# Optimization experiments

Measured on AMD Instinct MI355X. Metric: run time of the kernel, lower is better.

Reference implementation:

```python
import jax, jax.numpy as jnp
import numpy as np

BETA = 0.25  # commitment loss weight


def setup_inputs() -> dict:
    key = jax.random.key(0)
    k1, k2 = jax.random.split(key)
    x = jax.random.normal(k1, (16, 2048, 512), dtype=jnp.float32)          # [B, T, D]
    codebooks = jax.random.normal(k2, (8, 1024, 512), dtype=jnp.float32)   # [Q, C, D]
    return {"x": x, "codebooks": codebooks}


def reference(x, codebooks):
    """Residual VQ (SoundStream Algorithm 1): per stage, find nearest codebook
    entry to the current residual (squared-L2 cdist + argmin), gather the code,
    accumulate into the quantized output, subtract from the residual.
    Straight-through estimator on the quantize step; beta-weighted commit loss.
    """

    def step(carry, embed):
        residual, quantized_out, loss = carry  # residual: [B,T,D], embed: [C,D]
        # squared distances ||r - e||^2, GEMM-dominated: [B,T,C]
        d2 = (jnp.sum(residual * residual, axis=-1, keepdims=True)
              - 2.0 * jnp.einsum('btd,cd->btc', residual, embed)
              + jnp.sum(embed * embed, axis=-1))
        idx = jnp.argmin(d2, axis=-1)                 # [B,T] int32
        quant = embed[idx]                            # [B,T,D] gather
        # straight-through: forward value = quant, gradient = identity to residual
        quant_st = residual + jax.lax.stop_gradient(quant - residual)
        loss = loss + BETA * jnp.mean((residual - jax.lax.stop_gradient(quant)) ** 2)
        return (residual - quant_st, quantized_out + quant_st, loss), idx

    init = (x, jnp.zeros_like(x), jnp.float32(0.0))
    (_, quantized_out, loss), all_indices = jax.lax.scan(step, init, codebooks)
    # quantized_out: [B,T,D]; all_indices: [Q,B,T]; loss: scalar
    return quantized_out, all_indices, loss
```

## Files before the change

### kernel.cpp

```cpp
#include <hip/hip_runtime.h>

#define B_   16
#define T_   2048
#define D_   512
#define C_   1024
#define Q_   8
#define M_   (B_ * T_)
#define ND_  (M_ * D_)

static constexpr float BETA = 0.25f;

typedef short  short8v __attribute__((ext_vector_type(8)));
typedef short  short4v __attribute__((ext_vector_type(4)));
typedef float  f32x4   __attribute__((ext_vector_type(4)));

#define WS_CB16     0u
#define WS_ENORM    8388608u
#define WS_IDXI     8421376u
#define WS_FLAGS    8552448u
#define WS_CNT      8683520u
#define WS_NEED1    8683552u
#define WS_CB16LO   8683552u
#define WS_NEED2    17072160u
#define WS_CBT      17072384u
#define WS_NEED3    19169536u
#define WS_NEED3ALL 33849600u

__device__ __forceinline__ short f2bf(float f) {
    unsigned u = __float_as_uint(f);
    u += 0x7fffu + ((u >> 16) & 1u);
    return (short)(u >> 16);
}
__device__ __forceinline__ float bf2f(short s) {
    return __uint_as_float(((unsigned)(unsigned short)s) << 16);
}

__global__ __launch_bounds__(256) void k_enorm(const float* __restrict__ cb,
                                               float* __restrict__ enorm) {
    const int wave = threadIdx.x >> 6;
    const int lane = threadIdx.x & 63;
    const int code = blockIdx.x * 4 + wave;
    const float4* row = (const float4*)(cb + (size_t)code * D_);
    float s = 0.f;
    #pragma unroll
    for (int k = 0; k < 2; ++k) {
        float4 v = row[lane + k * 64];
        s += v.x * v.x + v.y * v.y + v.z * v.z + v.w * v.w;
    }
    #pragma unroll
    for (int m = 32; m; m >>= 1) s += __shfl_xor(s, m);
    if (lane == 0) enorm[code] = s;
}

__global__ __launch_bounds__(256) void k_cvt2f(const float* __restrict__ cb,
                                               short* __restrict__ hi,
                                               short* __restrict__ lo,
                                               int emit_lo) {
    const int idx8 = blockIdx.x * 256 + threadIdx.x;
    const int stage = idx8 >> 16;
    const int g = idx8 & 65535;
    const int lane = g & 63;
    const int h  = lane >> 4, lr = lane & 15;
    const int cj = (g >> 6) & 3;
    const int wc = (g >> 8) & 3;
    const int kb = (g >> 10) & 15;
    const int cc = (g >> 14) & 3;
    const int c  = cc * 256 + wc * 64 + cj * 16 + lr;
    const int ks = kb * 32 + h * 8;
    const float* src = cb + (size_t)stage * (C_ * D_) + (size_t)c * D_ + ks;
    float v[8];
    {
        float4 a = *(const float4*)(src);
        float4 b = *(const float4*)(src + 4);
        v[0]=a.x; v[1]=a.y; v[2]=a.z; v[3]=a.w;
        v[4]=b.x; v[5]=b.y; v[6]=b.z; v[7]=b.w;
    }
    short8v hv, lv;
    #pragma unroll
    for (int k = 0; k < 8; ++k) {
        hv[k] = f2bf(v[k]);
        lv[k] = f2bf(v[k] - bf2f(hv[k]));
    }
    const size_t dst = (size_t)stage * (C_ * D_) + (size_t)g * 8;
    *(short8v*)(hi + dst) = hv;
    if (emit_lo) *(short8v*)(lo + dst) = lv;
}

__global__ __launch_bounds__(64) void k_zero(float* __restrict__ loss,
                                             int* __restrict__ cnt) {
    if (threadIdx.x == 0) *loss = 0.f;
    if (threadIdx.x < 8) cnt[threadIdx.x] = 0;
}

__global__ __launch_bounds__(256)
void k_transpose(const float* __restrict__ cb0, float* __restrict__ cbT0) {
    __shared__ float tile[64][65];
    const float* cbq = cb0 + (size_t)blockIdx.z * C_ * D_;
    float* cbT = cbT0 + (size_t)blockIdx.z * C_ * D_;
    const int tid = threadIdx.x;
    const int c0 = blockIdx.x * 64;
    const int k0 = blockIdx.y * 64;
    #pragma unroll
    for (int i = 0; i < 4; ++i) {
        const int s = tid + i * 256;
        const int r = s >> 4, c4 = s & 15;
        const float4 v = *(const float4*)(cbq + (size_t)(c0 + r) * D_ + k0 + c4 * 4);
        tile[r][c4 * 4 + 0] = v.x; tile[r][c4 * 4 + 1] = v.y;
        tile[r][c4 * 4 + 2] = v.z; tile[r][c4 * 4 + 3] = v.w;
    }
    __syncthreads();
    #pragma unroll
    for (int i = 0; i < 4; ++i) {
        const int s = tid + i * 256;
        const int kk = s >> 4, cc4 = s & 15;
        float4 v;
        v.x = tile[cc4 * 4 + 0][kk]; v.y = tile[cc4 * 4 + 1][kk];
        v.z = tile[cc4 * 4 + 2][kk]; v.w = tile[cc4 * 4 + 3][kk];
        *(float4*)(cbT + (size_t)(k0 + kk) * C_ + c0 + cc4 * 4) = v;
    }
}

#define SA_OFF   0
#define MV1_OFF  131072
#define MV2_OFF  133120
#define MI1_OFF  135168
#define RED_OFF  137216
#define MROW_OFF 137248
#define SM_TOTAL 137760

template <int PLANES>
__global__ __launch_bounds__(512, 2)
void k_approx(const float* __restrict__ x,
              const float* __restrict__ cbprev,
              const short* __restrict__ cb16hi,
              const short* __restrict__ cb16lo,
              const float* __restrict__ enormq,
              float* __restrict__ qout,
              int*   __restrict__ idxi,
              float* __restrict__ idxf,
              int*   __restrict__ flaglist,
              int*   __restrict__ cnt,
              float* __restrict__ loss,
              int q) {
    __shared__ __align__(16) char smem[SM_TOTAL];
    short* smA  = (short*)(smem + SA_OFF);
    float* mv1  = (float*)(smem + MV1_OFF);
    float* mv2  = (float*)(smem + MV2_OFF);
    int*   mi1  = (int*)(smem + MI1_OFF);
    float* red  = (float*)(smem + RED_OFF);
    float* mrow = (float*)(smem + MROW_OFF);

    const int tid  = threadIdx.x;
    const int bid  = blockIdx.x;
    const int lane = tid & 63;
    const int w    = tid >> 6;
    const int rh   = w >> 2;
    const int wc   = w & 3;
    const int h    = lane >> 4;
    const int lr   = lane & 15;
    const int rbase = bid * 128;
    const float slope = (PLANES == 2) ? 0.002f : 0.05f;

    const int prow = tid >> 2;
    const int pqd  = tid & 3;
    const int grow1 = rbase + prow;
    float rn2 = 0.f, rlo2 = 0.f;
    int codep = 0;
    if (q > 0) codep = idxi[grow1];
    #pragma unroll 4
    for (int j = 0; j < 32; ++j) {
        const int c4 = pqd + j * 4;
        const size_t g = (size_t)grow1 * D_ + c4 * 4;
        const float4 xv = *(const float4*)(x + g);
        float4 r;
        if (q == 0) {
            r = xv;
        } else {
            const float4 ev = *(const float4*)(cbprev + (size_t)codep * D_ + c4 * 4);
            float4 nq;
            if (q == 1) nq = ev;
            else {
                const float4 qv = *(const float4*)(qout + g);
                nq = make_float4(qv.x + ev.x, qv.y + ev.y, qv.z + ev.z, qv.w + ev.w);
            }
            *(float4*)(qout + g) = nq;
            r = make_float4(xv.x - nq.x, xv.y - nq.y, xv.z - nq.z, xv.w - nq.w);
        }
        rn2 += r.x * r.x + r.y * r.y + r.z * r.z + r.w * r.w;
        short4v sv; sv[0]=f2bf(r.x); sv[1]=f2bf(r.y); sv[2]=f2bf(r.z); sv[3]=f2bf(r.w);
        const float dx = r.x - bf2f(sv[0]), dy = r.y - bf2f(sv[1]);
        const float dz = r.z - bf2f(sv[2]), dw = r.w - bf2f(sv[3]);
        rlo2 += dx * dx + dy * dy + dz * dz + dw * dw;
        int ab = (prow << 10) + (c4 << 3);
        ab ^= ((prow & 7) << 4);
        *(short4v*)((char*)smA + ab) = sv;
    }
    const float lpart = rn2;
    rn2  += __shfl_xor(rn2, 1);  rn2  += __shfl_xor(rn2, 2);
    rlo2 += __shfl_xor(rlo2, 1); rlo2 += __shfl_xor(rlo2, 2);
    if (pqd == 0)
        mrow[prow] = 32.f * sqrtf(rlo2) + slope * sqrtf(rn2) + 0.05f;
    __syncthreads();
    if (q != 0) {
        float lsum = lpart;
        #pragma unroll
        for (int m = 32; m; m >>= 1) lsum += __shfl_xor(lsum, m);
        if (lane == 0) red[w] = lsum;
        __syncthreads();
        if (tid == 0) {
            float t = 0.f;
            #pragma unroll
            for (int i = 0; i < 8; ++i) t += red[i];
            atomicAdd(loss, t * (BETA / (float)ND_));
        }
    }

    float v1[16], v2[16]; int i1[16];
    #pragma unroll
    for (int i = 0; i < 16; ++i) { v1[i] = 3.4e38f; v2[i] = 3.4e38f; i1[i] = 0; }

    auto bload = [&](const short* __restrict__ src, int cc, int kb, short8v* dst) {
        const short* p = src + (size_t)(((cc * 16 + kb) * 4 + wc) * 4) * 512 + lane * 8;
        #pragma unroll
        for (int cj = 0; cj < 4; ++cj)
            dst[cj] = *(const short8v*)(p + cj * 512);
    };

    short8v b0[4], b1[4];
    bload(cb16hi, 0, 0, b0);
    f32x4 acc[4][4];

    for (int cc = 0; cc < 4; ++cc) {
        #pragma unroll
        for (int ri = 0; ri < 4; ++ri)
            #pragma unroll
            for (int cj = 0; cj < 4; ++cj)
                acc[ri][cj] = (f32x4){0.f, 0.f, 0.f, 0.f};

        if (PLANES == 2) {
            for (int kb = 0; kb < 16; ++kb) {
                bload(cb16lo, cc, kb, b1);
                short8v a[4];
                const int kbyte = kb * 64 + h * 16;
                #pragma unroll
                for (int ri = 0; ri < 4; ++ri) {
                    const int row = rh * 64 + ri * 16 + lr;
                    int off = (row << 10) + kbyte;
                    off ^= ((row & 7) << 4);
                    a[ri] = *(const short8v*)((const char*)smA + off);
                }
                #pragma unroll
                for (int ri = 0; ri < 4; ++ri)
                    #pragma unroll
                    for (int cj = 0; cj < 4; ++cj)
                        acc[ri][cj] = __builtin_amdgcn_mfma_f32_16x16x32_bf16(a[ri], b0[cj], acc[ri][cj], 0, 0, 0);
                const int nkb = (kb == 15) ? 0 : kb + 1;
                const int ncc = (kb == 15) ? (cc < 3 ? cc + 1 : 3) : cc;
                bload(cb16hi, ncc, nkb, b0);
                #pragma unroll
                for (int ri = 0; ri < 4; ++ri)
                    #pragma unroll
                    for (int cj = 0; cj < 4; ++cj)
                        acc[ri][cj] = __builtin_amdgcn_mfma_f32_16x16x32_bf16(a[ri], b1[cj], acc[ri][cj], 0, 0, 0);
            }
        } else {
            for (int kb = 0; kb < 16; kb += 2) {
                {
                    short8v a[4];
                    const int kbyte = kb * 64 + h * 16;
                    #pragma unroll
                    for (int ri = 0; ri < 4; ++ri) {
                        const int row = rh * 64 + ri * 16 + lr;
                        int off = (row << 10) + kbyte;
                        off ^= ((row & 7) << 4);
                        a[ri] = *(const short8v*)((const char*)smA + off);
                    }
                    bload(cb16hi, cc, kb + 1, b1);
                    #pragma unroll
                    for (int ri = 0; ri < 4; ++ri)
                        #pragma unroll
                        for (int cj = 0; cj < 4; ++cj)
                            acc[ri][cj] = __builtin_amdgcn_mfma_f32_16x16x32_bf16(a[ri], b0[cj], acc[ri][cj], 0, 0, 0);
                }
                {
                    short8v a[4];
                    const int kbyte = (kb + 1) * 64 + h * 16;
                    #pragma unroll
                    for (int ri = 0; ri < 4; ++ri) {
                        const int row = rh * 64 + ri * 16 + lr;
                        int off = (row << 10) + kbyte;
                        off ^= ((row & 7) << 4);
                        a[ri] = *(const short8v*)((const char*)smA + off);
                    }
                    const int nkb = (kb == 14) ? 0 : kb + 2;
                    const int ncc = (kb == 14) ? (cc < 3 ? cc + 1 : 3) : cc;
                    bload(cb16hi, ncc, nkb, b0);
                    #pragma unroll
                    for (int ri = 0; ri < 4; ++ri)
                        #pragma unroll
                        for (int cj = 0; cj < 4; ++cj)
                            acc[ri][cj] = __builtin_amdgcn_mfma_f32_16x16x32_bf16(a[ri], b1[cj], acc[ri][cj], 0, 0, 0);
                }
            }
        }

        #pragma unroll
        for (int cj = 0; cj < 4; ++cj) {
            const int codeG = cc * 256 + wc * 64 + cj * 16 + lr;
            const float en = enormq[codeG];
            #pragma unroll
            for (int ri = 0; ri < 4; ++ri)
                #pragma unroll
                for (int rg = 0; rg < 4; ++rg) {
                    const float sv = fmaf(-2.f, acc[ri][cj][rg], en);
                    const int slot = ri * 4 + rg;
                    if (sv < v1[slot]) { v2[slot] = v1[slot]; v1[slot] = sv; i1[slot] = codeG; }
                    else               { v2[slot] = fminf(v2[slot], sv); }
                }
        }
    }

    #pragma unroll
    for (int slot = 0; slot < 16; ++slot) {
        float a1 = v1[slot], a2 = v2[slot]; int ai = i1[slot];
        #pragma unroll
        for (int m = 1; m < 16; m <<= 1) {
            const float b1m = __shfl_xor(a1, m);
            const int   bim = __shfl_xor(ai, m);
            const float b2m = __shfl_xor(a2, m);
            if (b1m < a1 || (b1m == a1 && bim < ai)) { a2 = fminf(a1, b2m); a1 = b1m; ai = bim; }
            else                                     { a2 = fminf(a2, b1m); }
        }
        v1[slot] = a1; v2[slot] = a2; i1[slot] = ai;
    }
    if (lr == 0) {
        #pragma unroll
        for (int ri = 0; ri < 4; ++ri)
            #pragma unroll
            for (int rg = 0; rg < 4; ++rg) {
                const int row = rh * 64 + ri * 16 + h * 4 + rg;
                mv1[wc * 128 + row] = v1[ri * 4 + rg];
                mv2[wc * 128 + row] = v2[ri * 4 + rg];
                mi1[wc * 128 + row] = i1[ri * 4 + rg];
            }
    }
    __syncthreads();

    if (tid < 128) {
        const int row = tid;
        float V1 = mv1[row]; int I1 = mi1[row]; float V2 = mv2[row];
        #pragma unroll
        for (int k = 1; k < 4; ++k) {
            const float b1m = mv1[k * 128 + row];
            const int   bim = mi1[k * 128 + row];
            const float b2m = mv2[k * 128 + row];
            if (b1m < V1 || (b1m == V1 && bim < I1)) { V2 = fminf(V1, b2m); V1 = b1m; I1 = bim; }
            else                                     { V2 = fminf(V2, b1m); }
        }
        const int grow = rbase + row;
        idxi[grow] = I1;
        idxf[grow] = (float)I1;
        if (!(V2 - V1 >= mrow[row])) {
            const int p = atomicAdd(cnt, 1);
            flaglist[p] = grow;
        }
    }
}

__global__ __launch_bounds__(256, 1)
void k_exact_t(const float* __restrict__ x, const float* __restrict__ qout,
               const float* __restrict__ cbT, const float* __restrict__ enq,
               int* __restrict__ idxi, float* __restrict__ idxf,
               const int* __restrict__ flaglist, const int* __restrict__ cnt,
               int useq) {
    __shared__ __align__(16) float rr[8][512];
    __shared__ int   rowid[8];
    __shared__ float wvv[8][4];
    __shared__ int   wii[8][4];
    const int tid  = threadIdx.x;
    const int lane = tid & 63;
    const int wv_  = tid >> 6;
    const int n = *cnt;
    const float4* cbT4 = (const float4*)cbT;

    for (int base = blockIdx.x * 8; base < n; base += gridDim.x * 8) {
        __syncthreads();
        if (tid < 8) rowid[tid] = (base + tid < n) ? flaglist[base + tid] : -1;
        __syncthreads();
        #pragma unroll
        for (int i = 0; i < 4; ++i) {
            const int s = tid + i * 256;
            const int j = s >> 7, k4 = s & 127;
            const int row = rowid[j];
            float4 v = make_float4(0.f, 0.f, 0.f, 0.f);
            if (row >= 0) {
                v = *(const float4*)(x + (size_t)row * D_ + k4 * 4);
                if (useq) {
                    const float4 qv = *(const float4*)(qout + (size_t)row * D_ + k4 * 4);
                    v = make_float4(v.x - qv.x, v.y - qv.y, v.z - qv.z, v.w - qv.w);
                }
            }
            *(float4*)&rr[j][k4 * 4] = v;
        }
        __syncthreads();

        float acc[8][4];
        #pragma unroll
        for (int j = 0; j < 8; ++j)
            #pragma unroll
            for (int c = 0; c < 4; ++c) acc[j][c] = 0.f;

        auto load16 = [&](float4* buf, int k0) {
            #pragma unroll
            for (int t = 0; t < 16; ++t)
                buf[t] = cbT4[(size_t)(k0 + t) * 256 + tid];
        };
        auto compute16 = [&](const float4* buf, int k0) {
            #pragma unroll
            for (int g = 0; g < 4; ++g) {
                const float4 e0 = buf[g * 4 + 0], e1 = buf[g * 4 + 1];
                const float4 e2 = buf[g * 4 + 2], e3 = buf[g * 4 + 3];
                #pragma unroll
                for (int j = 0; j < 8; ++j) {
                    const float4 rv = *(const float4*)&rr[j][k0 + g * 4];
                    acc[j][0] = fmaf(rv.x, e0.x, acc[j][0]);
                    acc[j][1] = fmaf(rv.x, e0.y, acc[j][1]);
                    acc[j][2] = fmaf(rv.x, e0.z, acc[j][2]);
                    acc[j][3] = fmaf(rv.x, e0.w, acc[j][3]);
                    acc[j][0] = fmaf(rv.y, e1.x, acc[j][0]);
                    acc[j][1] = fmaf(rv.y, e1.y, acc[j][1]);
                    acc[j][2] = fmaf(rv.y, e1.z, acc[j][2]);
                    acc[j][3] = fmaf(rv.y, e1.w, acc[j][3]);
                    acc[j][0] = fmaf(rv.z, e2.x, acc[j][0]);
                    acc[j][1] = fmaf(rv.z, e2.y, acc[j][1]);
                    acc[j][2] = fmaf(rv.z, e2.z, acc[j][2]);
                    acc[j][3] = fmaf(rv.z, e2.w, acc[j][3]);
                    acc[j][0] = fmaf(rv.w, e3.x, acc[j][0]);
                    acc[j][1] = fmaf(rv.w, e3.y, acc[j][1]);
                    acc[j][2] = fmaf(rv.w, e3.z, acc[j][2]);
                    acc[j][3] = fmaf(rv.w, e3.w, acc[j][3]);
                }
            }
        };

        float4 bufA[16], bufB[16];
        load16(bufA, 0);
        for (int ss = 0; ss < 32; ss += 2) {
            load16(bufB, (ss + 1) * 16);
            compute16(bufA, ss * 16);
            if (ss + 2 < 32) load16(bufA, (ss + 2) * 16);
            compute16(bufB, (ss + 1) * 16);
        }

        const float4 en4 = *(const float4*)(enq + tid * 4);
        #pragma unroll
        for (int j = 0; j < 8; ++j) {
            float v = 3.4e38f; int id = 0;
            {
                const float s0 = fmaf(-2.f, acc[j][0], en4.x);
                const float s1 = fmaf(-2.f, acc[j][1], en4.y);
                const float s2 = fmaf(-2.f, acc[j][2], en4.z);
                const float s3 = fmaf(-2.f, acc[j][3], en4.w);
                v = s0; id = tid * 4;
                if (s1 < v) { v = s1; id = tid * 4 + 1; }
                if (s2 < v) { v = s2; id = tid * 4 + 2; }
                if (s3 < v) { v = s3; id = tid * 4 + 3; }
            }
            #pragma unroll
            for (int m = 1; m < 64; m <<= 1) {
                const float ov = __shfl_xor(v, m);
                const int  oid = __shfl_xor(id, m);
                if (ov < v || (ov == v && oid < id)) { v = ov; id = oid; }
            }
            if (lane == 0) { wvv[j][wv_] = v; wii[j][wv_] = id; }
        }
        __syncthreads();
        if (tid < 8 && rowid[tid] >= 0) {
            float V = wvv[tid][0]; int I = wii[tid][0];
            #pragma unroll
            for (int k = 1; k < 4; ++k)
                if (wvv[tid][k] < V || (wvv[tid][k] == V && wii[tid][k] < I)) {
                    V = wvv[tid][k]; I = wii[tid][k];
                }
            idxi[rowid[tid]] = I;
            idxf[rowid[tid]] = (float)I;
        }
    }
}

#define XR 4
__global__ __launch_bounds__(256)
void k_exact(const float* __restrict__ x, const float* __restrict__ qout,
             const float* __restrict__ cbq, const float* __restrict__ enq,
             int* __restrict__ idxi, float* __restrict__ idxf,
             const int* __restrict__ flaglist, const int* __restrict__ cnt,
             int useq) {
    __shared__ float rr[XR][512];
    __shared__ int   rowid[XR];
    __shared__ float wv[4];
    __shared__ int   wi[4];
    const int tid = threadIdx.x;
    const int n = *cnt;
    for (int base = blockIdx.x * XR; base < n; base += gridDim.x * XR) {
        __syncthreads();
        if (tid < XR) rowid[tid] = (base + tid < n) ? flaglist[base + tid] : -1;
        __syncthreads();
        #pragma unroll
        for (int i = 0; i < 8; ++i) {
            const int s = tid + i * 256;
            const int j = s >> 9, k = s & 511;
            const int row = rowid[j];
            float v = 0.f;
            if (row >= 0) {
                v = x[(size_t)row * D_ + k];
                if (useq) v -= qout[(size_t)row * D_ + k];
            }
            rr[j][k] = v;
        }
        __syncthreads();
        float dotv[4][XR];
        #pragma unroll
        for (int cs = 0; cs < 4; ++cs)
            #pragma unroll
            for (int j = 0; j < XR; ++j) dotv[cs][j] = 0.f;
        for (int k4 = 0; k4 < 128; ++k4) {
            float4 rv[XR];
            #pragma unroll
            for (int j = 0; j < XR; ++j) rv[j] = *(const float4*)&rr[j][k4 * 4];
            #pragma unroll
            for (int cs = 0; cs < 4; ++cs) {
                const float4 e = *(const float4*)(cbq + (size_t)(cs * 256 + tid) * D_ + k4 * 4);
                #pragma unroll
                for (int j = 0; j < XR; ++j)
                    dotv[cs][j] = fmaf(e.x, rv[j].x, fmaf(e.y, rv[j].y,
                                  fmaf(e.z, rv[j].z, fmaf(e.w, rv[j].w, dotv[cs][j]))));
            }
        }
        float best[XR]; int bidx[XR];
        #pragma unroll
        for (int j = 0; j < XR; ++j) { best[j] = 3.4e38f; bidx[j] = 0; }
        #pragma unroll
        for (int cs = 0; cs < 4; ++cs) {
            const int c = cs * 256 + tid;
            const float en = enq[c];
            #pragma unroll
            for (int j = 0; j < XR; ++j) {
                const float sc = fmaf(-2.f, dotv[cs][j], en);
                if (sc < best[j]) { best[j] = sc; bidx[j] = c; }
            }
        }
        #pragma unroll
        for (int j = 0; j < XR; ++j) {
            float v = best[j]; int id = bidx[j];
            #pragma unroll
            for (int m = 1; m < 64; m <<= 1) {
                const float ov = __shfl_xor(v, m);
                const int  oid = __shfl_xor(id, m);
                if (ov < v || (ov == v && oid < id)) { v = ov; id = oid; }
            }
            if ((tid & 63) == 0) { wv[tid >> 6] = v; wi[tid >> 6] = id; }
            __syncthreads();
            if (tid == 0 && rowid[j] >= 0) {
                float V = wv[0]; int I = wi[0];
                #pragma unroll
                for (int k = 1; k < 4; ++k)
                    if (wv[k] < V || (wv[k] == V && wi[k] < I)) { V = wv[k]; I = wi[k]; }
                idxi[rowid[j]] = I;
                idxf[rowid[j]] = (float)I;
            }
            __syncthreads();
        }
    }
}

__global__ __launch_bounds__(256)
void k_final(const float* __restrict__ x, const float* __restrict__ cb7,
             const int* __restrict__ idxi, float* __restrict__ qout,
             float* __restrict__ loss) {
    __shared__ float red[4];
    const int tid = threadIdx.x;
    const int rbase = blockIdx.x * 64;
    float lsum = 0.f;
    for (int i = 0; i < 32; ++i) {
        const int s = tid + i * 256;
        const int row = s >> 7, c4 = s & 127;
        const int grow = rbase + row;
        const int code = idxi[grow];
        const float4 ev = *(const float4*)(cb7 + (size_t)code * D_ + c4 * 4);
        const size_t g = (size_t)grow * D_ + c4 * 4;
        const float4 xv = *(const float4*)(x + g);
        const float4 qv = *(const float4*)(qout + g);
        const float4 nq = make_float4(qv.x + ev.x, qv.y + ev.y, qv.z + ev.z, qv.w + ev.w);
        *(float4*)(qout + g) = nq;
        const float rx = xv.x - nq.x, ry = xv.y - nq.y;
        const float rz = xv.z - nq.z, rw = xv.w - nq.w;
        lsum += rx * rx + ry * ry + rz * rz + rw * rw;
    }
    #pragma unroll
    for (int m = 32; m; m >>= 1) lsum += __shfl_xor(lsum, m);
    if ((tid & 63) == 0) red[tid >> 6] = lsum;
    __syncthreads();
    if (tid == 0)
        atomicAdd(loss, (red[0] + red[1] + red[2] + red[3]) * (BETA / (float)ND_));
}

__global__ __launch_bounds__(256) void k_init(float* __restrict__ qout,
                                              float* __restrict__ loss) {
    const size_t tid = (size_t)blockIdx.x * blockDim.x + threadIdx.x;
    float4* q4 = (float4*)qout;
    const size_t n4 = ND_ / 4;
    for (size_t i = tid; i < n4; i += (size_t)gridDim.x * blockDim.x)
        q4[i] = make_float4(0.f, 0.f, 0.f, 0.f);
    if (tid == 0) *loss = 0.f;
}

__global__ __launch_bounds__(256) void k_stage(const float* __restrict__ x,
                                               const float* __restrict__ cb,
                                               const float* __restrict__ enorm,
                                               float* __restrict__ qout,
                                               float* __restrict__ idxf,
                                               float* __restrict__ loss) {
    __shared__ float As[16][68];
    __shared__ float Bs[16][68];
    __shared__ int   sidx[64];
    __shared__ float red[4];
    const int tid = threadIdx.x;
    const int ty  = tid >> 4;
    const int tx  = tid & 15;
    const int rbase = blockIdx.x * 64;
    const int lrow = tid >> 2;
    const int ld4  = tid & 3;
    float minv[4]; int mini[4];
    #pragma unroll
    for (int i = 0; i < 4; ++i) { minv[i] = 3.4e38f; mini[i] = 0; }
    for (int cchunk = 0; cchunk < 16; ++cchunk) {
        const int cbase = cchunk * 64;
        float acc[4][4] = {};
        for (int kb = 0; kb < D_; kb += 16) {
            __syncthreads();
            {
                const size_t g = (size_t)(rbase + lrow) * D_ + kb + ld4 * 4;
                const float4 xv = *(const float4*)(x + g);
                const float4 qv = *(const float4*)(qout + g);
                As[ld4*4+0][lrow] = xv.x - qv.x; As[ld4*4+1][lrow] = xv.y - qv.y;
                As[ld4*4+2][lrow] = xv.z - qv.z; As[ld4*4+3][lrow] = xv.w - qv.w;
                const size_t gb = (size_t)(cbase + lrow) * D_ + kb + ld4 * 4;
                const float4 bv = *(const float4*)(cb + gb);
                Bs[ld4*4+0][lrow] = bv.x; Bs[ld4*4+1][lrow] = bv.y;
                Bs[ld4*4+2][lrow] = bv.z; Bs[ld4*4+3][lrow] = bv.w;
            }
            __syncthreads();
            #pragma unroll
            for (int kk = 0; kk < 16; ++kk) {
                const float4 av = *(const float4*)&As[kk][ty * 4];
                const float4 bv = *(const float4*)&Bs[kk][tx * 4];
                const float a[4] = {av.x, av.y, av.z, av.w};
                const float b[4] = {bv.x, bv.y, bv.z, bv.w};
                #pragma unroll
                for (int i = 0; i < 4; ++i)
                    #pragma unroll
                    for (int j = 0; j < 4; ++j)
                        acc[i][j] = fmaf(a[i], b[j], acc[i][j]);
            }
        }
        #pragma unroll
        for (int j = 0; j < 4; ++j) {
            const int c = cbase + tx * 4 + j;
            const float en = enorm[c];
            #pragma unroll
            for (int i = 0; i < 4; ++i) {
                const float s = fmaf(-2.f, acc[i][j], en);
                if (s < minv[i]) { minv[i] = s; mini[i] = c; }
            }
        }
    }
    #pragma unroll
    for (int i = 0; i < 4; ++i) {
        float v = minv[i]; int id = mini[i];
        #pragma unroll
        for (int m = 1; m < 16; m <<= 1) {
            const float ov = __shfl_xor(v, m); const int oid = __shfl_xor(id, m);
            if (ov < v || (ov == v && oid < id)) { v = ov; id = oid; }
        }
        if (tx == 0) sidx[ty * 4 + i] = id;
    }
    __syncthreads();
    if (tid < 64) idxf[rbase + tid] = (float)sidx[tid];
    float lsum = 0.f;
    #pragma unroll 4
    for (int k = 0; k < 32; ++k) {
        const int fidx = tid + k * 256;
        const int row = fidx >> 7, c4 = fidx & 127;
        const int code = sidx[row];
        const float4 qv = *(const float4*)(cb + (size_t)code * D_ + c4 * 4);
        const size_t g = (size_t)(rbase + row) * D_ + c4 * 4;
        const float4 xv = *(const float4*)(x + g);
        const float4 ov = *(const float4*)(qout + g);
        const float4 nq = make_float4(ov.x + qv.x, ov.y + qv.y, ov.z + qv.z, ov.w + qv.w);
        *(float4*)(qout + g) = nq;
        const float rx = xv.x - nq.x, ry = xv.y - nq.y;
        const float rz = xv.z - nq.z, rw = xv.w - nq.w;
        lsum += rx * rx + ry * ry + rz * rz + rw * rw;
    }
    #pragma unroll
    for (int m = 32; m; m >>= 1) lsum += __shfl_xor(lsum, m);
    if ((tid & 63) == 0) red[tid >> 6] = lsum;
    __syncthreads();
    if (tid == 0)
        atomicAdd(loss, (red[0] + red[1] + red[2] + red[3]) * (BETA / (float)ND_));
}

extern "C" void kernel_launch(void* const* d_in, const int* in_sizes, int n_in,
                              void* d_out, int out_size, void* d_ws, size_t ws_size,
                              hipStream_t stream) {
    const float* x  = (const float*)d_in[0];
    const float* cb = (const float*)d_in[1];

    float* out  = (float*)d_out;
    float* qout = out;
    float* idxf = out + (size_t)ND_;
    float* loss = out + (size_t)ND_ + (size_t)Q_ * M_;

    if (ws_size >= WS_NEED1) {
        const bool twop   = (ws_size >= WS_NEED2);
        const bool hascbt = (ws_size >= WS_NEED3);
        const bool hasall = (ws_size >= WS_NEED3ALL);
        char*  ws    = (char*)d_ws;
        short* cb16  = (short*)(ws + WS_CB16);
        short* cb16l = (short*)(ws + WS_CB16LO);
        float* enorm = (float*)(ws + WS_ENORM);
        int*   idxi  = (int*)(ws + WS_IDXI);
        int*   flags = (int*)(ws + WS_FLAGS);
        int*   cnt   = (int*)(ws + WS_CNT);
        float* cbT   = (float*)(ws + WS_CBT);

        hipLaunchKernelGGL(k_zero, dim3(1), dim3(64), 0, stream, loss, cnt);
        hipLaunchKernelGGL(k_cvt2f, dim3(2048), dim3(256), 0, stream,
                           cb, cb16, twop ? cb16l : cb16, twop ? 1 : 0);
        hipLaunchKernelGGL(k_enorm, dim3((Q_ * C_) / 4), dim3(256), 0, stream, cb, enorm);
        if (hasall)
            hipLaunchKernelGGL(k_transpose, dim3(16, 8, 8), dim3(256), 0, stream, cb, cbT);

        for (int q = 0; q < Q_; ++q) {
            if (twop) {
                hipLaunchKernelGGL((k_approx<2>), dim3(M_ / 128), dim3(512), 0, stream,
                                   x, cb + (size_t)(q > 0 ? q - 1 : 0) * C_ * D_,
                                   cb16 + (size_t)q * C_ * D_,
                                   cb16l + (size_t)q * C_ * D_,
                                   enorm + (size_t)q * C_,
                                   qout, idxi, idxf + (size_t)q * M_,
                                   flags, cnt + q, loss, q);
            } else {
                hipLaunchKernelGGL((k_approx<1>), dim3(M_ / 128), dim3(512), 0, stream,
                                   x, cb + (size_t)(q > 0 ? q - 1 : 0) * C_ * D_,
                                   cb16 + (size_t)q * C_ * D_,
                                   cb16 + (size_t)q * C_ * D_,
                                   enorm + (size_t)q * C_,
                                   qout, idxi, idxf + (size_t)q * M_,
                                   flags, cnt + q, loss, q);
            }
            if (hascbt) {
                if (!hasall)
                    hipLaunchKernelGGL(k_transpose, dim3(16, 8, 1), dim3(256), 0, stream,
                                       cb + (size_t)q * C_ * D_, cbT);
                hipLaunchKernelGGL(k_exact_t, dim3(512), dim3(256), 0, stream,
                                   x, qout,
                                   hasall ? (cbT + (size_t)q * C_ * D_) : cbT,
                                   enorm + (size_t)q * C_,
                                   idxi, idxf + (size_t)q * M_,
                                   flags, cnt + q, q > 0 ? 1 : 0);
            } else {
                hipLaunchKernelGGL(k_exact, dim3(512), dim3(256), 0, stream,
                                   x, qout,
                                   cb + (size_t)q * C_ * D_,
                                   enorm + (size_t)q * C_,
                                   idxi, idxf + (size_t)q * M_,
                                   flags, cnt + q, q > 0 ? 1 : 0);
            }
        }
        hipLaunchKernelGGL(k_final, dim3(M_ / 64), dim3(256), 0, stream,
                           x, cb + (size_t)(Q_ - 1) * C_ * D_, idxi, qout, loss);
    } else {
        float* enorm = (float*)d_ws;
        hipLaunchKernelGGL(k_init, dim3(4096), dim3(256), 0, stream, qout, loss);
        hipLaunchKernelGGL(k_enorm, dim3((Q_ * C_) / 4), dim3(256), 0, stream, cb, enorm);
        for (int q = 0; q < Q_; ++q) {
            hipLaunchKernelGGL(k_stage, dim3(M_ / 64), dim3(256), 0, stream,
                               x, cb + (size_t)q * C_ * D_, enorm + (size_t)q * C_,
                               qout, idxf + (size_t)q * M_, loss);
        }
    }
}
```

Before: 1.537 ms.

## Replace two-plane bf16 distance GEMM with single-plane fp16 MFMA

The approximate distance pass switches from bf16 hi+lo split codebooks (two MFMA passes per k-block) to a single fp16 codebook plane and fp16 MFMA, halving the MFMA work and B-operand traffic. The candidate margin formula is retuned for fp16 rounding error so that fewer rows should be flagged for exact recompute. The exact fallback kernel's register double-buffer shrinks from 16 to 8 float4 per buffer and drops its occupancy bound. The risk is fp16 overflow or precision loss on large residuals, which would flag more rows for exact rescoring.

```diff
diff --git a/kernel.cpp b/kernel.cpp
--- a/kernel.cpp
+++ b/kernel.cpp
@@ -10,9 +10,11 @@
 
 static constexpr float BETA = 0.25f;
 
-typedef short  short8v __attribute__((ext_vector_type(8)));
-typedef short  short4v __attribute__((ext_vector_type(4)));
-typedef float  f32x4   __attribute__((ext_vector_type(4)));
+typedef short    short8v __attribute__((ext_vector_type(8)));
+typedef short    short4v __attribute__((ext_vector_type(4)));
+typedef _Float16 half8v  __attribute__((ext_vector_type(8)));
+typedef _Float16 half4v  __attribute__((ext_vector_type(4)));
+typedef float    f32x4   __attribute__((ext_vector_type(4)));
 
 #define WS_CB16     0u
 #define WS_ENORM    8388608u
@@ -20,20 +22,9 @@
 #define WS_FLAGS    8552448u
 #define WS_CNT      8683520u
 #define WS_NEED1    8683552u
-#define WS_CB16LO   8683552u
-#define WS_NEED2    17072160u
-#define WS_CBT      17072384u
-#define WS_NEED3    19169536u
-#define WS_NEED3ALL 33849600u
-
-__device__ __forceinline__ short f2bf(float f) {
-    unsigned u = __float_as_uint(f);
-    u += 0x7fffu + ((u >> 16) & 1u);
-    return (short)(u >> 16);
-}
-__device__ __forceinline__ float bf2f(short s) {
-    return __uint_as_float(((unsigned)(unsigned short)s) << 16);
-}
+#define WS_CBT      8683552u
+#define WS_NEED2    10780704u
+#define WS_NEED2ALL 25460768u
 
 __global__ __launch_bounds__(256) void k_enorm(const float* __restrict__ cb,
                                                float* __restrict__ enorm) {
@@ -52,10 +43,8 @@
     if (lane == 0) enorm[code] = s;
 }
 
-__global__ __launch_bounds__(256) void k_cvt2f(const float* __restrict__ cb,
-                                               short* __restrict__ hi,
-                                               short* __restrict__ lo,
-                                               int emit_lo) {
+__global__ __launch_bounds__(256) void k_cvtf16(const float* __restrict__ cb,
+                                                short* __restrict__ hi) {
     const int idx8 = blockIdx.x * 256 + threadIdx.x;
     const int stage = idx8 >> 16;
     const int g = idx8 & 65535;
@@ -75,15 +64,11 @@
         v[0]=a.x; v[1]=a.y; v[2]=a.z; v[3]=a.w;
         v[4]=b.x; v[5]=b.y; v[6]=b.z; v[7]=b.w;
     }
-    short8v hv, lv;
-    #pragma unroll
-    for (int k = 0; k < 8; ++k) {
-        hv[k] = f2bf(v[k]);
-        lv[k] = f2bf(v[k] - bf2f(hv[k]));
-    }
+    half8v hv;
+    #pragma unroll
+    for (int k = 0; k < 8; ++k) hv[k] = (_Float16)v[k];
     const size_t dst = (size_t)stage * (C_ * D_) + (size_t)g * 8;
-    *(short8v*)(hi + dst) = hv;
-    if (emit_lo) *(short8v*)(lo + dst) = lv;
+    *(half8v*)(hi + dst) = hv;
 }
 
 __global__ __launch_bounds__(64) void k_zero(float* __restrict__ loss,
@@ -128,12 +113,10 @@
 #define MROW_OFF 137248
 #define SM_TOTAL 137760
 
-template <int PLANES>
 __global__ __launch_bounds__(512, 2)
 void k_approx(const float* __restrict__ x,
               const float* __restrict__ cbprev,
-              const short* __restrict__ cb16hi,
-              const short* __restrict__ cb16lo,
+              const short* __restrict__ cb16,
               const float* __restrict__ enormq,
               float* __restrict__ qout,
               int*   __restrict__ idxi,
@@ -159,7 +142,6 @@
     const int h    = lane >> 4;
     const int lr   = lane & 15;
     const int rbase = bid * 128;
-    const float slope = (PLANES == 2) ? 0.002f : 0.05f;
 
     const int prow = tid >> 2;
     const int pqd  = tid & 3;
@@ -187,19 +169,21 @@
             r = make_float4(xv.x - nq.x, xv.y - nq.y, xv.z - nq.z, xv.w - nq.w);
         }
         rn2 += r.x * r.x + r.y * r.y + r.z * r.z + r.w * r.w;
-        short4v sv; sv[0]=f2bf(r.x); sv[1]=f2bf(r.y); sv[2]=f2bf(r.z); sv[3]=f2bf(r.w);
-        const float dx = r.x - bf2f(sv[0]), dy = r.y - bf2f(sv[1]);
-        const float dz = r.z - bf2f(sv[2]), dw = r.w - bf2f(sv[3]);
+        half4v hv;
+        hv[0] = (_Float16)r.x; hv[1] = (_Float16)r.y;
+        hv[2] = (_Float16)r.z; hv[3] = (_Float16)r.w;
+        const float dx = r.x - (float)hv[0], dy = r.y - (float)hv[1];
+        const float dz = r.z - (float)hv[2], dw = r.w - (float)hv[3];
         rlo2 += dx * dx + dy * dy + dz * dz + dw * dw;
         int ab = (prow << 10) + (c4 << 3);
         ab ^= ((prow & 7) << 4);
-        *(short4v*)((char*)smA + ab) = sv;
+        *(half4v*)((char*)smA + ab) = hv;
     }
     const float lpart = rn2;
     rn2  += __shfl_xor(rn2, 1);  rn2  += __shfl_xor(rn2, 2);
     rlo2 += __shfl_xor(rlo2, 1); rlo2 += __shfl_xor(rlo2, 2);
     if (pqd == 0)
-        mrow[prow] = 32.f * sqrtf(rlo2) + slope * sqrtf(rn2) + 0.05f;
+        mrow[prow] = 18.f * sqrtf(rlo2) + 0.005f * sqrtf(rn2) + 0.05f;
     __syncthreads();
     if (q != 0) {
         float lsum = lpart;
@@ -227,7 +211,7 @@
     };
 
     short8v b0[4], b1[4];
-    bload(cb16hi, 0, 0, b0);
+    bload(cb16, 0, 0, b0);
     f32x4 acc[4][4];
 
     for (int cc = 0; cc < 4; ++cc) {
@@ -237,9 +221,8 @@
             for (int cj = 0; cj < 4; ++cj)
                 acc[ri][cj] = (f32x4){0.f, 0.f, 0.f, 0.f};
 
-        if (PLANES == 2) {
-            for (int kb = 0; kb < 16; ++kb) {
-                bload(cb16lo, cc, kb, b1);
+        for (int kb = 0; kb < 16; kb += 2) {
+            {
                 short8v a[4];
                 const int kbyte = kb * 64 + h * 16;
                 #pragma unroll
@@ -249,58 +232,33 @@
                     off ^= ((row & 7) << 4);
                     a[ri] = *(const short8v*)((const char*)smA + off);
                 }
+                bload(cb16, cc, kb + 1, b1);
                 #pragma unroll
                 for (int ri = 0; ri < 4; ++ri)
                     #pragma unroll
                     for (int cj = 0; cj < 4; ++cj)
-                        acc[ri][cj] = __builtin_amdgcn_mfma_f32_16x16x32_bf16(a[ri], b0[cj], acc[ri][cj], 0, 0, 0);
-                const int nkb = (kb == 15) ? 0 : kb + 1;
-                const int ncc = (kb == 15) ? (cc < 3 ? cc + 1 : 3) : cc;
-                bload(cb16hi, ncc, nkb, b0);
+                        acc[ri][cj] = __builtin_amdgcn_mfma_f32_16x16x32_f16(
+                            *(half8v*)&a[ri], *(half8v*)&b0[cj], acc[ri][cj], 0, 0, 0);
+            }
+            {
+                short8v a[4];
+                const int kbyte = (kb + 1) * 64 + h * 16;
+                #pragma unroll
+                for (int ri = 0; ri < 4; ++ri) {
+                    const int row = rh * 64 + ri * 16 + lr;
+                    int off = (row << 10) + kbyte;
+                    off ^= ((row & 7) << 4);
+                    a[ri] = *(const short8v*)((const char*)smA + off);
+                }
+                const int nkb = (kb == 14) ? 0 : kb + 2;
+                const int ncc = (kb == 14) ? (cc < 3 ? cc + 1 : 3) : cc;
+                bload(cb16, ncc, nkb, b0);
                 #pragma unroll
                 for (int ri = 0; ri < 4; ++ri)
                     #pragma unroll
                     for (int cj = 0; cj < 4; ++cj)
-                        acc[ri][cj] = __builtin_amdgcn_mfma_f32_16x16x32_bf16(a[ri], b1[cj], acc[ri][cj], 0, 0, 0);
-            }
-        } else {
-            for (int kb = 0; kb < 16; kb += 2) {
-                {
-                    short8v a[4];
-                    const int kbyte = kb * 64 + h * 16;
-                    #pragma unroll
-                    for (int ri = 0; ri < 4; ++ri) {
-                        const int row = rh * 64 + ri * 16 + lr;
-                        int off = (row << 10) + kbyte;
-                        off ^= ((row & 7) << 4);
-                        a[ri] = *(const short8v*)((const char*)smA + off);
-                    }
-                    bload(cb16hi, cc, kb + 1, b1);
-                    #pragma unroll
-                    for (int ri = 0; ri < 4; ++ri)
-                        #pragma unroll
-                        for (int cj = 0; cj < 4; ++cj)
-                            acc[ri][cj] = __builtin_amdgcn_mfma_f32_16x16x32_bf16(a[ri], b0[cj], acc[ri][cj], 0, 0, 0);
-                }
-                {
-                    short8v a[4];
-                    const int kbyte = (kb + 1) * 64 + h * 16;
-                    #pragma unroll
-                    for (int ri = 0; ri < 4; ++ri) {
-                        const int row = rh * 64 + ri * 16 + lr;
-                        int off = (row << 10) + kbyte;
-                        off ^= ((row & 7) << 4);
-                        a[ri] = *(const short8v*)((const char*)smA + off);
-                    }
-                    const int nkb = (kb == 14) ? 0 : kb + 2;
-                    const int ncc = (kb == 14) ? (cc < 3 ? cc + 1 : 3) : cc;
-                    bload(cb16hi, ncc, nkb, b0);
-                    #pragma unroll
-                    for (int ri = 0; ri < 4; ++ri)
-                        #pragma unroll
-                        for (int cj = 0; cj < 4; ++cj)
-                            acc[ri][cj] = __builtin_amdgcn_mfma_f32_16x16x32_bf16(a[ri], b1[cj], acc[ri][cj], 0, 0, 0);
-                }
+                        acc[ri][cj] = __builtin_amdgcn_mfma_f32_16x16x32_f16(
+                            *(half8v*)&a[ri], *(half8v*)&b1[cj], acc[ri][cj], 0, 0, 0);
             }
         }
 
@@ -367,12 +325,12 @@
     }
 }
 
-__global__ __launch_bounds__(256, 1)
-void k_exact_t(const float* __restrict__ x, const float* __restrict__ qout,
-               const float* __restrict__ cbT, const float* __restrict__ enq,
-               int* __restrict__ idxi, float* __restrict__ idxf,
-               const int* __restrict__ flaglist, const int* __restrict__ cnt,
-               int useq) {
+__global__ __launch_bounds__(256)
+void k_exact3(const float* __restrict__ x, const float* __restrict__ qout,
+              const float* __restrict__ cbT, const float* __restrict__ enq,
+              int* __restrict__ idxi, float* __restrict__ idxf,
+              const int* __restrict__ flaglist, const int* __restrict__ cnt,
+              int useq) {
     __shared__ __align__(16) float rr[8][512];
     __shared__ int   rowid[8];
     __shared__ float wvv[8][4];
@@ -410,19 +368,21 @@
             #pragma unroll
             for (int c = 0; c < 4; ++c) acc[j][c] = 0.f;
 
-        auto load16 = [&](float4* buf, int k0) {
-            #pragma unroll
-            for (int t = 0; t < 16; ++t)
-                buf[t] = cbT4[(size_t)(k0 + t) * 256 + tid];
-        };
-        auto compute16 = [&](const float4* buf, int k0) {
-            #pragma unroll
-            for (int g = 0; g < 4; ++g) {
-                const float4 e0 = buf[g * 4 + 0], e1 = buf[g * 4 + 1];
-                const float4 e2 = buf[g * 4 + 2], e3 = buf[g * 4 + 3];
+        float4 bufA[8], bufB[8];
+        #pragma unroll
+        for (int t = 0; t < 8; ++t) bufA[t] = cbT4[(size_t)t * 256 + tid];
+
+        for (int g = 0; g < 64; g += 2) {
+            const int k0 = g * 8;
+            #pragma unroll
+            for (int t = 0; t < 8; ++t) bufB[t] = cbT4[(size_t)(k0 + 8 + t) * 256 + tid];
+            #pragma unroll
+            for (int kk = 0; kk < 8; kk += 4) {
                 #pragma unroll
                 for (int j = 0; j < 8; ++j) {
-                    const float4 rv = *(const float4*)&rr[j][k0 + g * 4];
+                    const float4 rv = *(const float4*)&rr[j][k0 + kk];
+                    const float4 e0 = bufA[kk + 0], e1 = bufA[kk + 1];
+                    const float4 e2 = bufA[kk + 2], e3 = bufA[kk + 3];
                     acc[j][0] = fmaf(rv.x, e0.x, acc[j][0]);
                     acc[j][1] = fmaf(rv.x, e0.y, acc[j][1]);
                     acc[j][2] = fmaf(rv.x, e0.z, acc[j][2]);
@@ -441,15 +401,35 @@
                     acc[j][3] = fmaf(rv.w, e3.w, acc[j][3]);
                 }
             }
-        };
-
-        float4 bufA[16], bufB[16];
-        load16(bufA, 0);
-        for (int ss = 0; ss < 32; ss += 2) {
-            load16(bufB, (ss + 1) * 16);
-            compute16(bufA, ss * 16);
-            if (ss + 2 < 32) load16(bufA, (ss + 2) * 16);
-            compute16(bufB, (ss + 1) * 16);
+            if (g + 2 < 64) {
+                #pragma unroll
+                for (int t = 0; t < 8; ++t) bufA[t] = cbT4[(size_t)(k0 + 16 + t) * 256 + tid];
+            }
+            #pragma unroll
+            for (int kk = 0; kk < 8; kk += 4) {
+                #pragma unroll
+                for (int j = 0; j < 8; ++j) {
+                    const float4 rv = *(const float4*)&rr[j][k0 + 8 + kk];
+                    const float4 e0 = bufB[kk + 0], e1 = bufB[kk + 1];
+                    const float4 e2 = bufB[kk + 2], e3 = bufB[kk + 3];
+                    acc[j][0] = fmaf(rv.x, e0.x, acc[j][0]);
+                    acc[j][1] = fmaf(rv.x, e0.y, acc[j][1]);
+                    acc[j][2] = fmaf(rv.x, e0.z, acc[j][2]);
+                    acc[j][3] = fmaf(rv.x, e0.w, acc[j][3]);
+                    acc[j][0] = fmaf(rv.y, e1.x, acc[j][0]);
+                    acc[j][1] = fmaf(rv.y, e1.y, acc[j][1]);
+                    acc[j][2] = fmaf(rv.y, e1.z, acc[j][2]);
+                    acc[j][3] = fmaf(rv.y, e1.w, acc[j][3]);
+                    acc[j][0] = fmaf(rv.z, e2.x, acc[j][0]);
+                    acc[j][1] = fmaf(rv.z, e2.y, acc[j][1]);
+                    acc[j][2] = fmaf(rv.z, e2.z, acc[j][2]);
+                    acc[j][3] = fmaf(rv.z, e2.w, acc[j][3]);
+                    acc[j][0] = fmaf(rv.w, e3.x, acc[j][0]);
+                    acc[j][1] = fmaf(rv.w, e3.y, acc[j][1]);
+                    acc[j][2] = fmaf(rv.w, e3.z, acc[j][2]);
+                    acc[j][3] = fmaf(rv.w, e3.w, acc[j][3]);
+                }
+            }
         }
 
         const float4 en4 = *(const float4*)(enq + tid * 4);
@@ -722,12 +702,10 @@
     float* loss = out + (size_t)ND_ + (size_t)Q_ * M_;
 
     if (ws_size >= WS_NEED1) {
-        const bool twop   = (ws_size >= WS_NEED2);
-        const bool hascbt = (ws_size >= WS_NEED3);
-        const bool hasall = (ws_size >= WS_NEED3ALL);
+        const bool hascbt = (ws_size >= WS_NEED2);
+        const bool hasall = (ws_size >= WS_NEED2ALL);
         char*  ws    = (char*)d_ws;
         short* cb16  = (short*)(ws + WS_CB16);
-        short* cb16l = (short*)(ws + WS_CB16LO);
         float* enorm = (float*)(ws + WS_ENORM);
         int*   idxi  = (int*)(ws + WS_IDXI);
         int*   flags = (int*)(ws + WS_FLAGS);
@@ -735,35 +713,23 @@
         float* cbT   = (float*)(ws + WS_CBT);
 
         hipLaunchKernelGGL(k_zero, dim3(1), dim3(64), 0, stream, loss, cnt);
-        hipLaunchKernelGGL(k_cvt2f, dim3(2048), dim3(256), 0, stream,
-                           cb, cb16, twop ? cb16l : cb16, twop ? 1 : 0);
+        hipLaunchKernelGGL(k_cvtf16, dim3(2048), dim3(256), 0, stream, cb, cb16);
         hipLaunchKernelGGL(k_enorm, dim3((Q_ * C_) / 4), dim3(256), 0, stream, cb, enorm);
         if (hasall)
             hipLaunchKernelGGL(k_transpose, dim3(16, 8, 8), dim3(256), 0, stream, cb, cbT);
 
         for (int q = 0; q < Q_; ++q) {
-            if (twop) {
-                hipLaunchKernelGGL((k_approx<2>), dim3(M_ / 128), dim3(512), 0, stream,
-                                   x, cb + (size_t)(q > 0 ? q - 1 : 0) * C_ * D_,
-                                   cb16 + (size_t)q * C_ * D_,
-                                   cb16l + (size_t)q * C_ * D_,
-                                   enorm + (size_t)q * C_,
-                                   qout, idxi, idxf + (size_t)q * M_,
-                                   flags, cnt + q, loss, q);
-            } else {
-                hipLaunchKernelGGL((k_approx<1>), dim3(M_ / 128), dim3(512), 0, stream,
-                                   x, cb + (size_t)(q > 0 ? q - 1 : 0) * C_ * D_,
-                                   cb16 + (size_t)q * C_ * D_,
-                                   cb16 + (size_t)q * C_ * D_,
-                                   enorm + (size_t)q * C_,
-                                   qout, idxi, idxf + (size_t)q * M_,
-                                   flags, cnt + q, loss, q);
-            }
+            hipLaunchKernelGGL(k_approx, dim3(M_ / 128), dim3(512), 0, stream,
+                               x, cb + (size_t)(q > 0 ? q - 1 : 0) * C_ * D_,
+                               cb16 + (size_t)q * C_ * D_,
+                               enorm + (size_t)q * C_,
+                               qout, idxi, idxf + (size_t)q * M_,
+                               flags, cnt + q, loss, q);
             if (hascbt) {
                 if (!hasall)
                     hipLaunchKernelGGL(k_transpose, dim3(16, 8, 1), dim3(256), 0, stream,
                                        cb + (size_t)q * C_ * D_, cbT);
-                hipLaunchKernelGGL(k_exact_t, dim3(512), dim3(256), 0, stream,
+                hipLaunchKernelGGL(k_exact3, dim3(512), dim3(256), 0, stream,
                                    x, qout,
                                    hasall ? (cbT + (size_t)q * C_ * D_) : cbT,
                                    enorm + (size_t)q * C_,
```

Measured after the change: 1.616 ms. 1.05x slower.
